# Optimization experiments

Measured on AMD Instinct MI355X. Metric: run time of the kernel, lower is better.

The kernel has to match this reference:

```python
import jax, jax.numpy as jnp
import numpy as np

RATIO = 0.25
RADIUS = 0.2
K = 32  # PyG radius() default max_num_neighbors


def fps(pos, n_samples):
    """Farthest point sampling for one cloud. pos: [N,3] -> indices [S]."""
    d2 = jnp.sum((pos - pos[0]) ** 2, axis=-1)  # dist to first (deterministic start)
    idx0 = jnp.zeros((n_samples,), jnp.int32)

    def body(i, state):
        idx, d = state
        nxt = jnp.argmax(d).astype(jnp.int32)
        idx = idx.at[i].set(nxt)
        d = jnp.minimum(d, jnp.sum((pos - pos[nxt]) ** 2, axis=-1))
        return idx, d

    idx, _ = jax.lax.fori_loop(1, n_samples, body, (idx0, d2))
    return idx


def setup_inputs() -> dict:
    key = jax.random.key(0)
    k0, k1, k2, k3 = jax.random.split(key, 4)
    B, N, C = 16, 4096, 64
    x = jax.random.normal(k0, (B, N, C), jnp.float32)
    pos = jax.random.uniform(k1, (B, N, 3), jnp.float32)  # unit cube
    W1 = jax.random.normal(k2, (C + 3, 128), jnp.float32) / np.sqrt(C + 3).astype(np.float32)
    b1 = jnp.zeros((128,), jnp.float32)
    W2 = jax.random.normal(k3, (128, 256), jnp.float32) / np.sqrt(128).astype(np.float32)
    b2 = jnp.zeros((256,), jnp.float32)
    return {"x": x, "pos": pos, "W1": W1, "b1": b1, "W2": W2, "b2": b2}


def reference(x, pos, W1, b1, W2, b2):
    B, N, C = x.shape
    S = int(N * RATIO)
    r2 = RADIUS * RADIUS

    # --- FPS per cloud ---
    samp = jax.vmap(lambda p: fps(p, S))(pos)            # [B,S] int32
    pos_s = jnp.take_along_axis(pos, samp[..., None], axis=1)  # [B,S,3]

    # --- ball query: K nearest within radius of each centroid ---
    d2 = jnp.sum((pos_s[:, :, None, :] - pos[:, None, :, :]) ** 2, axis=-1)  # [B,S,N]
    neg = jnp.where(d2 <= r2, -d2, -jnp.inf)
    negk, nbr = jax.lax.top_k(neg, K)                    # [B,S,K]
    valid = negk > -jnp.inf                              # centroid itself (d2=0) always valid

    # --- gather -> local MLP -> max pool (PointConv with max aggregation) ---
    x_j = jax.vmap(lambda xb, nb: xb[nb])(x, nbr)        # [B,S,K,C]
    pos_j = jax.vmap(lambda pb, nb: pb[nb])(pos, nbr)    # [B,S,K,3]
    rel = pos_j - pos_s[:, :, None, :]                   # pos_j - pos_i
    h = jnp.concatenate([x_j, rel], axis=-1)             # [B,S,K,C+3]
    h = jax.nn.relu(jnp.einsum("bskc,cd->bskd", h, W1) + b1)
    h = jax.nn.relu(jnp.einsum("bskd,de->bske", h, W2) + b2)
    h = jnp.where(valid[..., None], h, -jnp.inf)
    out = jnp.max(h, axis=2)                             # [B,S,256]
    return out, pos_s
```

## Files before the change

### kernel.cpp

```cpp
#include <hip/hip_runtime.h>
#include <stdint.h>

typedef unsigned short u16;
typedef unsigned int u32;
typedef unsigned long long u64;

#define NB 16
#define NP 4096
#define NCH 64
#define NS 1024
#define NK 32
#define H1D 128
#define H2D 256
#define KP1 96
#define LDA 104
#define LDH 136
#define OUTOFF (NB * NS * H2D)

typedef __attribute__((ext_vector_type(8))) short bfrag;
typedef __attribute__((ext_vector_type(4))) float facc4;

__device__ __forceinline__ u16 f2bf(float f) {
  u32 u = __float_as_uint(f);
  u += 0x7FFFu + ((u >> 16) & 1u);
  return (u16)(u >> 16);
}

__device__ __forceinline__ float dist2(float ax, float ay, float az,
                                       float bx, float by, float bz) {
#pragma clang fp contract(off)
  float dx = ax - bx, dy = ay - by, dz = az - bz;
  return dx * dx + dy * dy + dz * dz;
}

__device__ __forceinline__ float wave_max_f32(float v) {
  const int NI = (int)0xFF800000u;
  v = fmaxf(v, __int_as_float(__builtin_amdgcn_update_dpp(NI, __float_as_int(v), 0x111, 0xf, 0xf, false)));
  v = fmaxf(v, __int_as_float(__builtin_amdgcn_update_dpp(NI, __float_as_int(v), 0x112, 0xf, 0xf, false)));
  v = fmaxf(v, __int_as_float(__builtin_amdgcn_update_dpp(NI, __float_as_int(v), 0x114, 0xf, 0xf, false)));
  v = fmaxf(v, __int_as_float(__builtin_amdgcn_update_dpp(NI, __float_as_int(v), 0x118, 0xf, 0xf, false)));
  v = fmaxf(v, __int_as_float(__builtin_amdgcn_update_dpp(NI, __float_as_int(v), 0x142, 0xa, 0xf, false)));
  v = fmaxf(v, __int_as_float(__builtin_amdgcn_update_dpp(NI, __float_as_int(v), 0x143, 0xc, 0xf, false)));
  return __int_as_float(__builtin_amdgcn_readlane(__float_as_int(v), 63));
}

__device__ __forceinline__ u32 wave_min_u32(u32 v) {
  u32 t;
  t = (u32)__builtin_amdgcn_update_dpp(-1, (int)v, 0x111, 0xf, 0xf, false); v = t < v ? t : v;
  t = (u32)__builtin_amdgcn_update_dpp(-1, (int)v, 0x112, 0xf, 0xf, false); v = t < v ? t : v;
  t = (u32)__builtin_amdgcn_update_dpp(-1, (int)v, 0x114, 0xf, 0xf, false); v = t < v ? t : v;
  t = (u32)__builtin_amdgcn_update_dpp(-1, (int)v, 0x118, 0xf, 0xf, false); v = t < v ? t : v;
  t = (u32)__builtin_amdgcn_update_dpp(-1, (int)v, 0x142, 0xa, 0xf, false); v = t < v ? t : v;
  t = (u32)__builtin_amdgcn_update_dpp(-1, (int)v, 0x143, 0xc, 0xf, false); v = t < v ? t : v;
  return (u32)__builtin_amdgcn_readlane((int)v, 63);
}

__global__ void setup_kernel(const float* __restrict__ W1, const float* __restrict__ W2,
                             u16* __restrict__ W1T, u16* __restrict__ W2T) {
  int idx = blockIdx.x * 256 + threadIdx.x;
  if (idx < H1D * KP1) {
    int n = idx / KP1, k = idx % KP1;
    W1T[idx] = f2bf(k < 67 ? W1[k * H1D + n] : 0.f);
  } else if (idx < H1D * KP1 + H2D * H1D) {
    int j = idx - H1D * KP1;
    int n = j / H1D, k = j % H1D;
    W2T[j] = f2bf(W2[k * H2D + n]);
  }
}

__global__ __launch_bounds__(256) void fps_kernel(const float* __restrict__ pos,
                                                  int* __restrict__ samp,
                                                  float* __restrict__ pos_s) {
  __shared__ float4 plds[NP];
  __shared__ __align__(16) u64 wkey[2][4];
  const int b = blockIdx.x;
  const int tid = threadIdx.x;
  const int lane = tid & 63, wv = tid >> 6;
  const float* pb = pos + (size_t)b * NP * 3;
  for (int k = tid; k < NP; k += 256)
    plds[k] = make_float4(pb[k * 3 + 0], pb[k * 3 + 1], pb[k * 3 + 2], 0.f);
  __syncthreads();

  float px[16], py[16], pz[16], d[16];
  const float4 q0 = plds[0];
  float bv = -1.f;
  int bj = 0;
#pragma unroll
  for (int j = 0; j < 16; ++j) {
    const float4 p4 = plds[j * 256 + tid];
    px[j] = p4.x; py[j] = p4.y; pz[j] = p4.z;
    d[j] = dist2(p4.x, p4.y, p4.z, q0.x, q0.y, q0.z);
    const bool cg = d[j] > bv;
    bv = cg ? d[j] : bv;
    bj = cg ? j : bj;
  }
  if (tid == 0) {
    samp[b * NS] = 0;
    pos_s[(size_t)b * NS * 3 + 0] = q0.x;
    pos_s[(size_t)b * NS * 3 + 1] = q0.y;
    pos_s[(size_t)b * NS * 3 + 2] = q0.z;
  }

  for (int i = 1; i < NS; ++i) {
    const float wmax = wave_max_f32(bv);
    const u32 cand = (bv == wmax) ? (u32)(bj * 256 + tid) : 0xFFFFFFFFu;
    const u32 widx = wave_min_u32(cand);
    if (lane == 0)
      wkey[i & 1][wv] = ((u64)__float_as_uint(wmax) << 32) | (u64)(4095u - widx);
    __syncthreads();
    const ulonglong2 k01 = *(const ulonglong2*)&wkey[i & 1][0];
    const ulonglong2 k23 = *(const ulonglong2*)&wkey[i & 1][2];
    u64 g = k01.x;
    g = k01.y > g ? k01.y : g;
    g = k23.x > g ? k23.x : g;
    g = k23.y > g ? k23.y : g;
    const int gi = __builtin_amdgcn_readfirstlane(4095 - (int)((u32)g & 0xFFFu));
    const float4 q = plds[gi];
    if (tid == 0) {
      samp[b * NS + i] = gi;
      pos_s[((size_t)b * NS + i) * 3 + 0] = q.x;
      pos_s[((size_t)b * NS + i) * 3 + 1] = q.y;
      pos_s[((size_t)b * NS + i) * 3 + 2] = q.z;
    }
    bv = -1.f; bj = 0;
#pragma unroll
    for (int j = 0; j < 16; ++j) {
      d[j] = fminf(d[j], dist2(px[j], py[j], pz[j], q.x, q.y, q.z));
      const bool cg = d[j] > bv;
      bv = cg ? d[j] : bv;
      bj = cg ? j : bj;
    }
  }
}

__global__ __launch_bounds__(256) void ballq_kernel(const float* __restrict__ pos,
                                                    const int* __restrict__ samp,
                                                    int* __restrict__ nbr) {
  __shared__ u64 buf[4][256];
  const int lane = threadIdx.x & 63, wv = threadIdx.x >> 6;
  const int sg = blockIdx.x * 4 + wv;
  const int b = sg >> 10;
  const int nc = samp[sg];
  const float* pb = pos + (size_t)b * NP * 3;
  const float cx = pb[nc * 3 + 0], cy = pb[nc * 3 + 1], cz = pb[nc * 3 + 2];
  const float r2 = (float)(0.2 * 0.2);
  int V = 0;
  for (int c = 0; c < 64; ++c) {
    const int i = c * 64 + lane;
    const float d2v = dist2(cx, cy, cz, pb[i * 3 + 0], pb[i * 3 + 1], pb[i * 3 + 2]);
    const bool valid = d2v <= r2;
    const u64 bal = __ballot(valid);
    if (valid) {
      const int rank = __popcll(bal & ((1ull << lane) - 1ull));
      const int p = V + rank;
      if (p < 256) buf[wv][p] = ((u64)__float_as_uint(d2v) << 32) | (u32)i;
    }
    V += __popcll(bal);
  }
  if (V > 256) V = 256;
  u32 kd[4], ki[4];
#pragma unroll
  for (int t = 0; t < 4; ++t) {
    const int p = t * 64 + lane;
    const u64 v = (p < V) ? buf[wv][p] : ~0ull;
    kd[t] = (u32)(v >> 32);
    ki[t] = (u32)v;
  }
  u32 my = 0, pad = 0;
  for (int e = 0; e < 32; ++e) {
    u32 m0 = kd[0] < kd[1] ? kd[0] : kd[1];
    u32 m1 = kd[2] < kd[3] ? kd[2] : kd[3];
    const u32 m = wave_min_u32(m0 < m1 ? m0 : m1);
    u32 ci = 0xFFFFFFFFu;
#pragma unroll
    for (int t = 0; t < 4; ++t) {
      const u32 cm = (ki[t] < ci) ? ki[t] : ci;
      ci = (kd[t] == m) ? cm : ci;
    }
    const u32 wi = wave_min_u32(ci);
    if (e == 0) pad = wi;
    const u32 sel = (m == 0xFFFFFFFFu) ? pad : wi;
    if (lane == e) my = sel;
#pragma unroll
    for (int t = 0; t < 4; ++t)
      if (ki[t] == wi) kd[t] = 0xFFFFFFFFu;
  }
  if (lane < 32) nbr[(size_t)sg * NK + lane] = (int)my;
}

__global__ __launch_bounds__(256) void mlp_kernel(
    const float* __restrict__ x, const float* __restrict__ pos,
    const float* __restrict__ b1, const float* __restrict__ b2,
    const int* __restrict__ nbr, const u16* __restrict__ W1T,
    const u16* __restrict__ W2T, const float* __restrict__ pos_s,
    float* __restrict__ out) {
  __shared__ u16 A[128 * LDA];
  __shared__ u16 Hs[128 * LDH];
  const int ctr0 = blockIdx.x * 4;
  const int b = ctr0 >> 10;
  const int tid = threadIdx.x;
  {
    const int row = tid >> 1, half = tid & 1;
    const int g = ctr0 + (row >> 5);
    const int n = nbr[(size_t)g * NK + (row & 31)];
    const float4* xr = (const float4*)(x + ((size_t)b * NP + n) * NCH + half * 32);
#pragma unroll
    for (int qq = 0; qq < 4; ++qq) {
      const float4 v0 = xr[2 * qq], v1 = xr[2 * qq + 1];
      uint4 wp;
      wp.x = (u32)f2bf(v0.x) | ((u32)f2bf(v0.y) << 16);
      wp.y = (u32)f2bf(v0.z) | ((u32)f2bf(v0.w) << 16);
      wp.z = (u32)f2bf(v1.x) | ((u32)f2bf(v1.y) << 16);
      wp.w = (u32)f2bf(v1.z) | ((u32)f2bf(v1.w) << 16);
      *(uint4*)&A[row * LDA + half * 32 + qq * 8] = wp;
    }
    if (half == 0) {
      const float rx = pos[((size_t)b * NP + n) * 3 + 0] - pos_s[(size_t)g * 3 + 0];
      const float ry = pos[((size_t)b * NP + n) * 3 + 1] - pos_s[(size_t)g * 3 + 1];
      const float rz = pos[((size_t)b * NP + n) * 3 + 2] - pos_s[(size_t)g * 3 + 2];
      uint4 wr;
      wr.x = (u32)f2bf(rx) | ((u32)f2bf(ry) << 16);
      wr.y = (u32)f2bf(rz);
      wr.z = 0; wr.w = 0;
      uint4 wz;
      wz.x = wz.y = wz.z = wz.w = 0;
      *(uint4*)&A[row * LDA + 64] = wr;
      *(uint4*)&A[row * LDA + 72] = wz;
      *(uint4*)&A[row * LDA + 80] = wz;
      *(uint4*)&A[row * LDA + 88] = wz;
    }
  }
  __syncthreads();
  const int lane = tid & 63, w = tid >> 6;
  const int r16 = lane & 15, g4 = lane >> 4;
  {
    bfrag af[2][3];
#pragma unroll
    for (int mg2 = 0; mg2 < 2; ++mg2)
#pragma unroll
      for (int ks = 0; ks < 3; ++ks)
        af[mg2][ks] = *(const bfrag*)&A[((2 * w + mg2) * 16 + r16) * LDA + ks * 32 + g4 * 8];
#pragma unroll
    for (int ng = 0; ng < 8; ++ng) {
      const bfrag bw0 = *(const bfrag*)&W1T[(ng * 16 + r16) * KP1 + 0 + g4 * 8];
      const bfrag bw1 = *(const bfrag*)&W1T[(ng * 16 + r16) * KP1 + 32 + g4 * 8];
      const bfrag bw2 = *(const bfrag*)&W1T[(ng * 16 + r16) * KP1 + 64 + g4 * 8];
      facc4 a0 = {0.f, 0.f, 0.f, 0.f}, a1 = {0.f, 0.f, 0.f, 0.f};
      a0 = __builtin_amdgcn_mfma_f32_16x16x32_bf16(bw0, af[0][0], a0, 0, 0, 0);
      a0 = __builtin_amdgcn_mfma_f32_16x16x32_bf16(bw1, af[0][1], a0, 0, 0, 0);
      a0 = __builtin_amdgcn_mfma_f32_16x16x32_bf16(bw2, af[0][2], a0, 0, 0, 0);
      a1 = __builtin_amdgcn_mfma_f32_16x16x32_bf16(bw0, af[1][0], a1, 0, 0, 0);
      a1 = __builtin_amdgcn_mfma_f32_16x16x32_bf16(bw1, af[1][1], a1, 0, 0, 0);
      a1 = __builtin_amdgcn_mfma_f32_16x16x32_bf16(bw2, af[1][2], a1, 0, 0, 0);
      const float4 bias4 = *(const float4*)&b1[ng * 16 + g4 * 4];
      const int nb = ng * 16 + g4 * 4;
      u32 lo0 = (u32)f2bf(fmaxf(a0[0] + bias4.x, 0.f)) | ((u32)f2bf(fmaxf(a0[1] + bias4.y, 0.f)) << 16);
      u32 hi0 = (u32)f2bf(fmaxf(a0[2] + bias4.z, 0.f)) | ((u32)f2bf(fmaxf(a0[3] + bias4.w, 0.f)) << 16);
      u32 lo1 = (u32)f2bf(fmaxf(a1[0] + bias4.x, 0.f)) | ((u32)f2bf(fmaxf(a1[1] + bias4.y, 0.f)) << 16);
      u32 hi1 = (u32)f2bf(fmaxf(a1[2] + bias4.z, 0.f)) | ((u32)f2bf(fmaxf(a1[3] + bias4.w, 0.f)) << 16);
      *(uint2*)&Hs[((2 * w + 0) * 16 + r16) * LDH + nb] = make_uint2(lo0, hi0);
      *(uint2*)&Hs[((2 * w + 1) * 16 + r16) * LDH + nb] = make_uint2(lo1, hi1);
    }
  }
  __syncthreads();
  {
    bfrag hf[2][4];
#pragma unroll
    for (int mg2 = 0; mg2 < 2; ++mg2)
#pragma unroll
      for (int ks = 0; ks < 4; ++ks)
        hf[mg2][ks] = *(const bfrag*)&Hs[((2 * w + mg2) * 16 + r16) * LDH + ks * 32 + g4 * 8];
    const int gout = ctr0 + w;
    const int NI = (int)0xFF800000u;
#pragma unroll
    for (int ng = 0; ng < 16; ++ng) {
      facc4 a0 = {0.f, 0.f, 0.f, 0.f}, a1 = {0.f, 0.f, 0.f, 0.f};
#pragma unroll
      for (int ks = 0; ks < 4; ++ks) {
        const bfrag bw = *(const bfrag*)&W2T[(ng * 16 + r16) * H1D + ks * 32 + g4 * 8];
        a0 = __builtin_amdgcn_mfma_f32_16x16x32_bf16(bw, hf[0][ks], a0, 0, 0, 0);
        a1 = __builtin_amdgcn_mfma_f32_16x16x32_bf16(bw, hf[1][ks], a1, 0, 0, 0);
      }
      float v0 = fmaxf(a0[0], a1[0]);
      float v1 = fmaxf(a0[1], a1[1]);
      float v2 = fmaxf(a0[2], a1[2]);
      float v3 = fmaxf(a0[3], a1[3]);
#pragma unroll
      for (int s = 0; s < 4; ++s) {
        const int ctrl = 0x111 << s ? 0 : 0;
        (void)ctrl;
      }
      v0 = fmaxf(v0, __int_as_float(__builtin_amdgcn_update_dpp(NI, __float_as_int(v0), 0x111, 0xf, 0xf, false)));
      v1 = fmaxf(v1, __int_as_float(__builtin_amdgcn_update_dpp(NI, __float_as_int(v1), 0x111, 0xf, 0xf, false)));
      v2 = fmaxf(v2, __int_as_float(__builtin_amdgcn_update_dpp(NI, __float_as_int(v2), 0x111, 0xf, 0xf, false)));
      v3 = fmaxf(v3, __int_as_float(__builtin_amdgcn_update_dpp(NI, __float_as_int(v3), 0x111, 0xf, 0xf, false)));
      v0 = fmaxf(v0, __int_as_float(__builtin_amdgcn_update_dpp(NI, __float_as_int(v0), 0x112, 0xf, 0xf, false)));
      v1 = fmaxf(v1, __int_as_float(__builtin_amdgcn_update_dpp(NI, __float_as_int(v1), 0x112, 0xf, 0xf, false)));
      v2 = fmaxf(v2, __int_as_float(__builtin_amdgcn_update_dpp(NI, __float_as_int(v2), 0x112, 0xf, 0xf, false)));
      v3 = fmaxf(v3, __int_as_float(__builtin_amdgcn_update_dpp(NI, __float_as_int(v3), 0x112, 0xf, 0xf, false)));
      v0 = fmaxf(v0, __int_as_float(__builtin_amdgcn_update_dpp(NI, __float_as_int(v0), 0x114, 0xf, 0xf, false)));
      v1 = fmaxf(v1, __int_as_float(__builtin_amdgcn_update_dpp(NI, __float_as_int(v1), 0x114, 0xf, 0xf, false)));
      v2 = fmaxf(v2, __int_as_float(__builtin_amdgcn_update_dpp(NI, __float_as_int(v2), 0x114, 0xf, 0xf, false)));
      v3 = fmaxf(v3, __int_as_float(__builtin_amdgcn_update_dpp(NI, __float_as_int(v3), 0x114, 0xf, 0xf, false)));
      v0 = fmaxf(v0, __int_as_float(__builtin_amdgcn_update_dpp(NI, __float_as_int(v0), 0x118, 0xf, 0xf, false)));
      v1 = fmaxf(v1, __int_as_float(__builtin_amdgcn_update_dpp(NI, __float_as_int(v1), 0x118, 0xf, 0xf, false)));
      v2 = fmaxf(v2, __int_as_float(__builtin_amdgcn_update_dpp(NI, __float_as_int(v2), 0x118, 0xf, 0xf, false)));
      v3 = fmaxf(v3, __int_as_float(__builtin_amdgcn_update_dpp(NI, __float_as_int(v3), 0x118, 0xf, 0xf, false)));
      if ((lane & 15) == 15) {
        const float4 b24 = *(const float4*)&b2[ng * 16 + g4 * 4];
        float4 o;
        o.x = fmaxf(v0 + b24.x, 0.f);
        o.y = fmaxf(v1 + b24.y, 0.f);
        o.z = fmaxf(v2 + b24.z, 0.f);
        o.w = fmaxf(v3 + b24.w, 0.f);
        *(float4*)&out[(size_t)gout * H2D + ng * 16 + g4 * 4] = o;
      }
    }
  }
}

extern "C" void kernel_launch(void* const* d_in, const int* in_sizes, int n_in,
                              void* d_out, int out_size, void* d_ws, size_t ws_size,
                              hipStream_t stream) {
  const float* x = (const float*)d_in[0];
  const float* pos = (const float*)d_in[1];
  const float* W1 = (const float*)d_in[2];
  const float* b1 = (const float*)d_in[3];
  const float* W2 = (const float*)d_in[4];
  const float* b2 = (const float*)d_in[5];
  float* out = (float*)d_out;
  char* ws = (char*)d_ws;
  u16* W1T = (u16*)(ws + 0);
  u16* W2T = (u16*)(ws + 24576);
  int* samp = (int*)(ws + 90112);
  int* nbr = (int*)(ws + 155648);
  float* pos_s = out + OUTOFF;

  setup_kernel<<<dim3(176), dim3(256), 0, stream>>>(W1, W2, W1T, W2T);
  fps_kernel<<<dim3(NB), dim3(256), 0, stream>>>(pos, samp, pos_s);
  ballq_kernel<<<dim3(NB * NS / 4), dim3(256), 0, stream>>>(pos, samp, nbr);
  mlp_kernel<<<dim3(NB * NS / 4), dim3(256), 0, stream>>>(x, pos, b1, b2, nbr, W1T, W2T,
                                                          pos_s, out);
}
```

Before: 921.9 us.

## Streamline FPS argmax: ballot winner, broadcast position records, packed f32x2 distances

```diff
diff --git a/kernel.cpp b/kernel.cpp
--- a/kernel.cpp
+++ b/kernel.cpp
@@ -19,6 +19,7 @@
 
 typedef __attribute__((ext_vector_type(8))) short bfrag;
 typedef __attribute__((ext_vector_type(4))) float facc4;
+typedef __attribute__((ext_vector_type(2))) float f32x2;
 
 __device__ __forceinline__ u16 f2bf(float f) {
   u32 u = __float_as_uint(f);
@@ -30,6 +31,13 @@
                                        float bx, float by, float bz) {
 #pragma clang fp contract(off)
   float dx = ax - bx, dy = ay - by, dz = az - bz;
+  return dx * dx + dy * dy + dz * dz;
+}
+
+__device__ __forceinline__ f32x2 dist2v(f32x2 ax, f32x2 ay, f32x2 az,
+                                        float bx, float by, float bz) {
+#pragma clang fp contract(off)
+  f32x2 dx = ax - bx, dy = ay - by, dz = az - bz;
   return dx * dx + dy * dy + dz * dz;
 }
 
@@ -54,6 +62,18 @@
   t = (u32)__builtin_amdgcn_update_dpp(-1, (int)v, 0x143, 0xc, 0xf, false); v = t < v ? t : v;
   return (u32)__builtin_amdgcn_readlane((int)v, 63);
 }
+
+#define QUAD_MAX_STEP(CTRL)                                                           \
+  {                                                                                   \
+    const u32 plo = (u32)__builtin_amdgcn_update_dpp(0, (int)klo, (CTRL), 0xf, 0xf, true); \
+    const u32 phi = (u32)__builtin_amdgcn_update_dpp(0, (int)khi, (CTRL), 0xf, 0xf, true); \
+    const u32 pqx = (u32)__builtin_amdgcn_update_dpp(0, (int)qxu, (CTRL), 0xf, 0xf, true); \
+    const u32 pqy = (u32)__builtin_amdgcn_update_dpp(0, (int)qyu, (CTRL), 0xf, 0xf, true); \
+    const u32 pqz = (u32)__builtin_amdgcn_update_dpp(0, (int)qzu, (CTRL), 0xf, 0xf, true); \
+    const u64 ok = ((u64)phi << 32) | plo;                                            \
+    const u64 mk = ((u64)khi << 32) | klo;                                            \
+    if (ok > mk) { klo = plo; khi = phi; qxu = pqx; qyu = pqy; qzu = pqz; }           \
+  }
 
 __global__ void setup_kernel(const float* __restrict__ W1, const float* __restrict__ W2,
                              u16* __restrict__ W1T, u16* __restrict__ W2T) {
@@ -72,7 +92,7 @@
                                                   int* __restrict__ samp,
                                                   float* __restrict__ pos_s) {
   __shared__ float4 plds[NP];
-  __shared__ __align__(16) u64 wkey[2][4];
+  __shared__ __align__(16) u32 recs[2][4][8];
   const int b = blockIdx.x;
   const int tid = threadIdx.x;
   const int lane = tid & 63, wv = tid >> 6;
@@ -81,18 +101,21 @@
     plds[k] = make_float4(pb[k * 3 + 0], pb[k * 3 + 1], pb[k * 3 + 2], 0.f);
   __syncthreads();
 
-  float px[16], py[16], pz[16], d[16];
+  f32x2 px2[8], py2[8], pz2[8], dd[8];
   const float4 q0 = plds[0];
   float bv = -1.f;
   int bj = 0;
 #pragma unroll
-  for (int j = 0; j < 16; ++j) {
-    const float4 p4 = plds[j * 256 + tid];
-    px[j] = p4.x; py[j] = p4.y; pz[j] = p4.z;
-    d[j] = dist2(p4.x, p4.y, p4.z, q0.x, q0.y, q0.z);
-    const bool cg = d[j] > bv;
-    bv = cg ? d[j] : bv;
-    bj = cg ? j : bj;
+  for (int t = 0; t < 8; ++t) {
+    const float4 pA = plds[tid * 16 + 2 * t];
+    const float4 pB = plds[tid * 16 + 2 * t + 1];
+    px2[t] = (f32x2){pA.x, pB.x};
+    py2[t] = (f32x2){pA.y, pB.y};
+    pz2[t] = (f32x2){pA.z, pB.z};
+    const f32x2 s = dist2v(px2[t], py2[t], pz2[t], q0.x, q0.y, q0.z);
+    dd[t] = s;
+    const bool c0 = s.x > bv; bv = c0 ? s.x : bv; bj = c0 ? 2 * t : bj;
+    const bool c1 = s.y > bv; bv = c1 ? s.y : bv; bj = c1 ? 2 * t + 1 : bj;
   }
   if (tid == 0) {
     samp[b * NS] = 0;
@@ -102,33 +125,40 @@
   }
 
   for (int i = 1; i < NS; ++i) {
+    const int gidx = tid * 16 + bj;
+    const float4 cpos = plds[gidx];
     const float wmax = wave_max_f32(bv);
-    const u32 cand = (bv == wmax) ? (u32)(bj * 256 + tid) : 0xFFFFFFFFu;
-    const u32 widx = wave_min_u32(cand);
-    if (lane == 0)
-      wkey[i & 1][wv] = ((u64)__float_as_uint(wmax) << 32) | (u64)(4095u - widx);
+    const u64 mask = __ballot(bv == wmax);
+    const bool winner = (bv == wmax) && ((mask & ((1ull << lane) - 1ull)) == 0ull);
+    if (winner) {
+      u32* rp = &recs[i & 1][wv][0];
+      *(uint4*)rp = make_uint4(4095u - (u32)gidx, __float_as_uint(bv),
+                               __float_as_uint(cpos.x), __float_as_uint(cpos.y));
+      rp[4] = __float_as_uint(cpos.z);
+    }
     __syncthreads();
-    const ulonglong2 k01 = *(const ulonglong2*)&wkey[i & 1][0];
-    const ulonglong2 k23 = *(const ulonglong2*)&wkey[i & 1][2];
-    u64 g = k01.x;
-    g = k01.y > g ? k01.y : g;
-    g = k23.x > g ? k23.x : g;
-    g = k23.y > g ? k23.y : g;
-    const int gi = __builtin_amdgcn_readfirstlane(4095 - (int)((u32)g & 0xFFFu));
-    const float4 q = plds[gi];
+    const u32* sp = &recs[i & 1][lane & 3][0];
+    const uint4 rA = *(const uint4*)sp;
+    u32 klo = rA.x, khi = rA.y, qxu = rA.z, qyu = rA.w, qzu = sp[4];
+    QUAD_MAX_STEP(0xB1)
+    QUAD_MAX_STEP(0x4E)
+    const float qx = __uint_as_float(qxu);
+    const float qy = __uint_as_float(qyu);
+    const float qz = __uint_as_float(qzu);
     if (tid == 0) {
-      samp[b * NS + i] = gi;
-      pos_s[((size_t)b * NS + i) * 3 + 0] = q.x;
-      pos_s[((size_t)b * NS + i) * 3 + 1] = q.y;
-      pos_s[((size_t)b * NS + i) * 3 + 2] = q.z;
+      samp[b * NS + i] = 4095 - (int)(klo & 0xFFFu);
+      pos_s[((size_t)b * NS + i) * 3 + 0] = qx;
+      pos_s[((size_t)b * NS + i) * 3 + 1] = qy;
+      pos_s[((size_t)b * NS + i) * 3 + 2] = qz;
     }
     bv = -1.f; bj = 0;
 #pragma unroll
-    for (int j = 0; j < 16; ++j) {
-      d[j] = fminf(d[j], dist2(px[j], py[j], pz[j], q.x, q.y, q.z));
-      const bool cg = d[j] > bv;
-      bv = cg ? d[j] : bv;
-      bj = cg ? j : bj;
+    for (int t = 0; t < 8; ++t) {
+      const f32x2 s = dist2v(px2[t], py2[t], pz2[t], qx, qy, qz);
+      dd[t].x = fminf(dd[t].x, s.x);
+      dd[t].y = fminf(dd[t].y, s.y);
+      const bool c0 = dd[t].x > bv; bv = c0 ? dd[t].x : bv; bj = c0 ? 2 * t : bj;
+      const bool c1 = dd[t].y > bv; bv = c1 ? dd[t].y : bv; bj = c1 ? 2 * t + 1 : bj;
     }
   }
 }
@@ -285,11 +315,6 @@
       float v1 = fmaxf(a0[1], a1[1]);
       float v2 = fmaxf(a0[2], a1[2]);
       float v3 = fmaxf(a0[3], a1[3]);
-#pragma unroll
-      for (int s = 0; s < 4; ++s) {
-        const int ctrl = 0x111 << s ? 0 : 0;
-        (void)ctrl;
-      }
       v0 = fmaxf(v0, __int_as_float(__builtin_amdgcn_update_dpp(NI, __float_as_int(v0), 0x111, 0xf, 0xf, false)));
       v1 = fmaxf(v1, __int_as_float(__builtin_amdgcn_update_dpp(NI, __float_as_int(v1), 0x111, 0xf, 0xf, false)));
       v2 = fmaxf(v2, __int_as_float(__builtin_amdgcn_update_dpp(NI, __float_as_int(v2), 0x111, 0xf, 0xf, false)));
```

After: 917.8 us. No clear change (-0.4%).

## Double FPS block to 512 threads and use packed float2 distance math

Applied to the files above, without the earlier changes.

```diff
diff --git a/kernel.cpp b/kernel.cpp
--- a/kernel.cpp
+++ b/kernel.cpp
@@ -19,6 +19,7 @@
 
 typedef __attribute__((ext_vector_type(8))) short bfrag;
 typedef __attribute__((ext_vector_type(4))) float facc4;
+typedef __attribute__((ext_vector_type(2))) float f32x2;
 
 __device__ __forceinline__ u16 f2bf(float f) {
   u32 u = __float_as_uint(f);
@@ -30,6 +31,13 @@
                                        float bx, float by, float bz) {
 #pragma clang fp contract(off)
   float dx = ax - bx, dy = ay - by, dz = az - bz;
+  return dx * dx + dy * dy + dz * dz;
+}
+
+__device__ __forceinline__ f32x2 dist2v(f32x2 ax, f32x2 ay, f32x2 az,
+                                        float bx, float by, float bz) {
+#pragma clang fp contract(off)
+  f32x2 dx = ax - bx, dy = ay - by, dz = az - bz;
   return dx * dx + dy * dy + dz * dz;
 }
 
@@ -68,31 +76,34 @@
   }
 }
 
-__global__ __launch_bounds__(256) void fps_kernel(const float* __restrict__ pos,
+__global__ __launch_bounds__(512) void fps_kernel(const float* __restrict__ pos,
                                                   int* __restrict__ samp,
                                                   float* __restrict__ pos_s) {
   __shared__ float4 plds[NP];
-  __shared__ __align__(16) u64 wkey[2][4];
+  __shared__ __align__(16) u64 wkey[2][8];
   const int b = blockIdx.x;
   const int tid = threadIdx.x;
   const int lane = tid & 63, wv = tid >> 6;
   const float* pb = pos + (size_t)b * NP * 3;
-  for (int k = tid; k < NP; k += 256)
+  for (int k = tid; k < NP; k += 512)
     plds[k] = make_float4(pb[k * 3 + 0], pb[k * 3 + 1], pb[k * 3 + 2], 0.f);
   __syncthreads();
 
-  float px[16], py[16], pz[16], d[16];
+  f32x2 px2[4], py2[4], pz2[4], dd[4];
   const float4 q0 = plds[0];
   float bv = -1.f;
   int bj = 0;
 #pragma unroll
-  for (int j = 0; j < 16; ++j) {
-    const float4 p4 = plds[j * 256 + tid];
-    px[j] = p4.x; py[j] = p4.y; pz[j] = p4.z;
-    d[j] = dist2(p4.x, p4.y, p4.z, q0.x, q0.y, q0.z);
-    const bool cg = d[j] > bv;
-    bv = cg ? d[j] : bv;
-    bj = cg ? j : bj;
+  for (int t = 0; t < 4; ++t) {
+    const float4 pA = plds[(2 * t) * 512 + tid];
+    const float4 pB = plds[(2 * t + 1) * 512 + tid];
+    px2[t] = (f32x2){pA.x, pB.x};
+    py2[t] = (f32x2){pA.y, pB.y};
+    pz2[t] = (f32x2){pA.z, pB.z};
+    const f32x2 s = dist2v(px2[t], py2[t], pz2[t], q0.x, q0.y, q0.z);
+    dd[t] = s;
+    const bool c0 = s.x > bv; bv = c0 ? s.x : bv; bj = c0 ? 2 * t : bj;
+    const bool c1 = s.y > bv; bv = c1 ? s.y : bv; bj = c1 ? 2 * t + 1 : bj;
   }
   if (tid == 0) {
     samp[b * NS] = 0;
@@ -103,18 +114,23 @@
 
   for (int i = 1; i < NS; ++i) {
     const float wmax = wave_max_f32(bv);
-    const u32 cand = (bv == wmax) ? (u32)(bj * 256 + tid) : 0xFFFFFFFFu;
+    const u32 cand = (bv == wmax) ? (u32)(bj * 512 + tid) : 0xFFFFFFFFu;
     const u32 widx = wave_min_u32(cand);
     if (lane == 0)
       wkey[i & 1][wv] = ((u64)__float_as_uint(wmax) << 32) | (u64)(4095u - widx);
     __syncthreads();
     const ulonglong2 k01 = *(const ulonglong2*)&wkey[i & 1][0];
     const ulonglong2 k23 = *(const ulonglong2*)&wkey[i & 1][2];
-    u64 g = k01.x;
-    g = k01.y > g ? k01.y : g;
-    g = k23.x > g ? k23.x : g;
-    g = k23.y > g ? k23.y : g;
-    const int gi = __builtin_amdgcn_readfirstlane(4095 - (int)((u32)g & 0xFFFu));
+    const ulonglong2 k45 = *(const ulonglong2*)&wkey[i & 1][4];
+    const ulonglong2 k67 = *(const ulonglong2*)&wkey[i & 1][6];
+    u64 g0 = k01.x > k01.y ? k01.x : k01.y;
+    u64 g1 = k23.x > k23.y ? k23.x : k23.y;
+    u64 g2 = k45.x > k45.y ? k45.x : k45.y;
+    u64 g3 = k67.x > k67.y ? k67.x : k67.y;
+    g0 = g1 > g0 ? g1 : g0;
+    g2 = g3 > g2 ? g3 : g2;
+    g0 = g2 > g0 ? g2 : g0;
+    const int gi = __builtin_amdgcn_readfirstlane(4095 - (int)((u32)g0 & 0xFFFu));
     const float4 q = plds[gi];
     if (tid == 0) {
       samp[b * NS + i] = gi;
@@ -124,11 +140,12 @@
     }
     bv = -1.f; bj = 0;
 #pragma unroll
-    for (int j = 0; j < 16; ++j) {
-      d[j] = fminf(d[j], dist2(px[j], py[j], pz[j], q.x, q.y, q.z));
-      const bool cg = d[j] > bv;
-      bv = cg ? d[j] : bv;
-      bj = cg ? j : bj;
+    for (int t = 0; t < 4; ++t) {
+      const f32x2 s = dist2v(px2[t], py2[t], pz2[t], q.x, q.y, q.z);
+      dd[t].x = fminf(dd[t].x, s.x);
+      dd[t].y = fminf(dd[t].y, s.y);
+      const bool c0 = dd[t].x > bv; bv = c0 ? dd[t].x : bv; bj = c0 ? 2 * t : bj;
+      const bool c1 = dd[t].y > bv; bv = c1 ? dd[t].y : bv; bj = c1 ? 2 * t + 1 : bj;
     }
   }
 }
@@ -285,11 +302,6 @@
       float v1 = fmaxf(a0[1], a1[1]);
       float v2 = fmaxf(a0[2], a1[2]);
       float v3 = fmaxf(a0[3], a1[3]);
-#pragma unroll
-      for (int s = 0; s < 4; ++s) {
-        const int ctrl = 0x111 << s ? 0 : 0;
-        (void)ctrl;
-      }
       v0 = fmaxf(v0, __int_as_float(__builtin_amdgcn_update_dpp(NI, __float_as_int(v0), 0x111, 0xf, 0xf, false)));
       v1 = fmaxf(v1, __int_as_float(__builtin_amdgcn_update_dpp(NI, __float_as_int(v1), 0x111, 0xf, 0xf, false)));
       v2 = fmaxf(v2, __int_as_float(__builtin_amdgcn_update_dpp(NI, __float_as_int(v2), 0x111, 0xf, 0xf, false)));
@@ -337,7 +349,7 @@
   float* pos_s = out + OUTOFF;
 
   setup_kernel<<<dim3(176), dim3(256), 0, stream>>>(W1, W2, W1T, W2T);
-  fps_kernel<<<dim3(NB), dim3(256), 0, stream>>>(pos, samp, pos_s);
+  fps_kernel<<<dim3(NB), dim3(512), 0, stream>>>(pos, samp, pos_s);
   ballq_kernel<<<dim3(NB * NS / 4), dim3(256), 0, stream>>>(pos, samp, nbr);
   mlp_kernel<<<dim3(NB * NS / 4), dim3(256), 0, stream>>>(x, pos, b1, b2, nbr, W1T, W2T,
                                                           pos_s, out);
```

Measured after the change: 945.2 us. 1.03x slower.
